# Performance work log

Measured on AMD Instinct MI355X. Metric: run time of the kernel, lower is better.

## Reference

```python
import jax, jax.numpy as jnp
import numpy as np

SCALE = 4.0
GRID = 64
B, T, A, C = 4, 256, 3, 13
F = 5 + C  # x,y,z,r,conf,cls...


def setup_inputs() -> dict:
    key = jax.random.key(0)
    k1, k2, k3, k4, k5 = jax.random.split(key, 5)
    p = jax.random.normal(k1, (B, A, GRID, GRID, GRID, F), dtype=jnp.float32)
    xyz = jax.random.uniform(k2, (B, T, 3), minval=4.0, maxval=SCALE * GRID - 4.0)
    r = jax.random.uniform(k3, (B, T, 1), minval=6.0, maxval=20.0)
    conf = (jax.random.uniform(k4, (B, T, 1)) < 0.6).astype(jnp.float32)
    cls = jax.nn.one_hot(jax.random.randint(k5, (B, T), 0, C), C, dtype=jnp.float32)
    targets = jnp.concatenate([xyz, r, conf, cls], axis=-1)  # [B,T,18]
    anchor = jnp.array([[[8.0], [12.0], [16.0]]], dtype=jnp.float32)  # [1,A,1]
    return {"p": p, "targets": targets, "anchor": anchor}


def _bce(logits, t):
    # BCEWithLogitsLoss (pos_weight=1), elementwise
    return t * jax.nn.softplus(-logits) + (1.0 - t) * jax.nn.softplus(logits)


def _eiou(box1, box2, eps=1e-7):
    # boxes are (x,y,z,r): axis-aligned cubes of side r centered at xyz (3D EIoU)
    c1, r1 = box1[:, :3], box1[:, 3]
    c2, r2 = box2[:, :3], box2[:, 3]
    h1, h2 = r1[:, None] * 0.5, r2[:, None] * 0.5
    lo = jnp.maximum(c1 - h1, c2 - h2)
    hi = jnp.minimum(c1 + h1, c2 + h2)
    inter = jnp.prod(jnp.clip(hi - lo, 0.0), axis=-1)
    union = r1 ** 3 + r2 ** 3 - inter + eps
    iou = inter / union
    clo = jnp.minimum(c1 - h1, c2 - h2)
    chi = jnp.maximum(c1 + h1, c2 + h2)
    cdim = chi - clo  # enclosing box per-axis extent
    rho2 = jnp.sum((c1 - c2) ** 2, axis=-1)
    c2diag = jnp.sum(cdim ** 2, axis=-1) + eps
    size_pen = jnp.sum(((r1 - r2) ** 2)[:, None] / (cdim ** 2 + eps), axis=-1)
    return iou - rho2 / c2diag - size_pen


def reference(p, targets, anchor):
    Bs, An, K, J, I, Fd = p.shape
    Cn = Fd - 5
    g, gr = 0.5, 0.0
    Tn = targets.shape[1]
    n = Bs * Tn
    x = targets.reshape(n, Fd)
    b0 = jnp.repeat(jnp.arange(Bs), Tn)
    conf_m = x[:, 4] > 0.5
    anchor_norm = anchor[0] / SCALE  # [A,1]
    gxyzr = x[:, :4] / SCALE
    rn = gxyzr[:, 3]
    ratio = rn[None, :] / anchor_norm  # [A,n]
    aok = jnp.maximum(ratio, 1.0 / ratio) < 4.0
    gxyz = gxyzr[:, :3]
    gdim = jnp.array([K, J, I], dtype=p.dtype)  # gain[1:]
    gxyz_i = gdim - gxyz
    m1 = (gxyz % 1.0 < g) & (gxyz > 1.0)
    m2 = (gxyz_i % 1.0 < g) & (gxyz_i > 1.0)
    fm = jnp.stack([jnp.ones_like(m1[:, 0]), m1[:, 0], m1[:, 1], m1[:, 2], m2[:, 0], m2[:, 1], m2[:, 2]])  # [7,n]
    off = jnp.array([[0, 0, 0], [1, 0, 0], [0, 1, 0], [0, 0, 1], [-1, 0, 0], [0, -1, 0], [0, 0, -1]], dtype=p.dtype) * g
    valid = (conf_m[None, None, :] & aok[None, :, :] & fm[:, None, :]).reshape(-1)  # [7*A*n]
    bidx = jnp.broadcast_to(b0[None, None, :], (7, An, n)).reshape(-1)
    aidx = jnp.broadcast_to(jnp.arange(An)[None, :, None], (7, An, n)).reshape(-1)
    gxyz_c = jnp.broadcast_to(gxyz[None, None], (7, An, n, 3))
    off_c = jnp.broadcast_to(off[:, None, None, :], (7, An, n, 3))
    gijk_f = jnp.trunc(jax.lax.stop_gradient(gxyz_c - off_c))  # torch .long() truncates
    gijk = gijk_f.astype(jnp.int32).reshape(-1, 3)
    gi = jnp.clip(gijk[:, 0], 0, I - 1)
    gj = jnp.clip(gijk[:, 1], 0, J - 1)
    gk = jnp.clip(gijk[:, 2], 0, K - 1)
    tbox = jnp.concatenate([(gxyz_c - gijk_f).reshape(-1, 3), jnp.broadcast_to(rn[None, None, :], (7, An, n)).reshape(-1, 1)], axis=1)
    anchors = anchor_norm[aidx]  # [N,1]
    tcls = jnp.broadcast_to(x[None, None, :, 5:], (7, An, n, Cn)).reshape(-1, Cn)
    pred = p[bidx, aidx, gk, gj, gi]  # [N,F]
    pxyz = jax.nn.sigmoid(pred[:, :3]) * 2.0 - 0.5
    pr = (jax.nn.sigmoid(pred[:, 3:4]) * 2.0) ** 2 * anchors
    pbox = jnp.concatenate([pxyz, pr], axis=1)
    ei = _eiou(pbox, tbox)
    w = valid.astype(p.dtype)
    nv = jnp.maximum(jnp.sum(w), 1.0)
    loss_bbox = jnp.sum(w * (1.0 - ei)) / nv  # masked mean == torch mean over filtered rows
    iou_d = jax.lax.stop_gradient(jnp.clip(ei, 0.0))
    objv = (1.0 - gr) + gr * iou_d  # gr=0 -> 1.0
    tobj = jnp.zeros((Bs, An, K, J, I), dtype=p.dtype).at[bidx, aidx, gk, gj, gi].max(w * objv)
    loss_cls = jnp.sum(w[:, None] * _bce(pred[:, 5:], tcls)) / (nv * Cn)
    loss_obj = jnp.mean(_bce(p[..., 4], tobj))
    lb = loss_bbox * 1.0
    lo = loss_obj * 20.0
    lc = loss_cls * 10.0
    return ((lb + lo + lc) * Bs, lo, lc)
```

## Files before the change

### kernel.cpp

```cpp
#include <hip/hip_runtime.h>
#include <math.h>

#define NTGT   1024
#define NCAND  (21 * NTGT)
#define NCBLK  (NCAND / 256)
#define NCELL  (4 * 3 * 64 * 64 * 64)
#define BITW   (NCELL / 32)
#define NBLK   2048

__device__ __forceinline__ float softplusf(float x) {
    return fmaxf(x, 0.0f) + __logf(1.0f + __expf(-fabsf(x)));
}
__device__ __forceinline__ float sigmoidf(float x) {
    return 1.0f / (1.0f + __expf(-x));
}

__global__ __launch_bounds__(256) void fused_kernel(
    const float* __restrict__ p, const float* __restrict__ tg,
    const float* __restrict__ anchor, float* __restrict__ acc,
    unsigned int* __restrict__ bitmap)
{
    if (blockIdx.x < NCBLK) {
        int idx = blockIdx.x * 256 + threadIdx.x;
        float nv_v = 0.f, bb_v = 0.f, cl_v = 0.f, ob_v = 0.f;
        {
            int t  = idx & (NTGT - 1);
            int oa = idx >> 10;
            int a  = oa % 3;
            int o  = oa / 3;
            const float* x = tg + t * 18;
            float conf = x[4];
            float rn   = x[3] * 0.25f;
            float an   = anchor[a] * 0.25f;
            float ratio = rn / an;
            bool ok = (conf > 0.5f) && (fmaxf(ratio, 1.0f / ratio) < 4.0f);
            float gv[3] = { x[0] * 0.25f, x[1] * 0.25f, x[2] * 0.25f };
            float off[3] = { 0.f, 0.f, 0.f };
            if (o >= 1) {
                if (o <= 3) {
                    int c = o - 1;
                    float v = gv[c];
                    ok = ok && ((v - floorf(v)) < 0.5f) && (v > 1.0f);
                    off[c] = 0.5f;
                } else {
                    int c = o - 4;
                    float vi = 64.0f - gv[c];
                    ok = ok && ((vi - floorf(vi)) < 0.5f) && (vi > 1.0f);
                    off[c] = -0.5f;
                }
            }
            if (ok) {
                float tb[3]; int gq[3];
                #pragma unroll
                for (int c = 0; c < 3; c++) {
                    float f = truncf(gv[c] - off[c]);
                    tb[c] = gv[c] - f;
                    gq[c] = min(max((int)f, 0), 63);
                }
                int b0 = t >> 8;
                unsigned int cell =
                    ((((unsigned)(b0 * 3 + a) * 64u + (unsigned)gq[2]) * 64u
                      + (unsigned)gq[1]) * 64u) + (unsigned)gq[0];
                const float* pp = p + (size_t)cell * 18u;
                float pd[18];
                #pragma unroll
                for (int f = 0; f < 18; f++) pd[f] = pp[f];

                float c1[3];
                #pragma unroll
                for (int c = 0; c < 3; c++) c1[c] = sigmoidf(pd[c]) * 2.0f - 0.5f;
                float s4 = sigmoidf(pd[3]) * 2.0f;
                float r1 = s4 * s4 * an;
                float r2 = rn;

                float h1 = 0.5f * r1, h2 = 0.5f * r2;
                float inter = 1.f, rho2 = 0.f, c2d = 0.f, spen = 0.f;
                float dr2 = (r1 - r2) * (r1 - r2);
                #pragma unroll
                for (int c = 0; c < 3; c++) {
                    float lo1 = c1[c] - h1, hi1 = c1[c] + h1;
                    float lo2 = tb[c] - h2, hi2 = tb[c] + h2;
                    inter *= fmaxf(fminf(hi1, hi2) - fmaxf(lo1, lo2), 0.f);
                    float cd  = fmaxf(hi1, hi2) - fminf(lo1, lo2);
                    float cd2 = cd * cd;
                    float d   = c1[c] - tb[c];
                    rho2 += d * d;
                    c2d  += cd2;
                    spen += dr2 / (cd2 + 1e-7f);
                }
                float uni = r1 * r1 * r1 + r2 * r2 * r2 - inter + 1e-7f;
                float ei  = inter / uni - rho2 / (c2d + 1e-7f) - spen;

                nv_v = 1.0f;
                bb_v = 1.0f - ei;
                float cl = 0.f;
                #pragma unroll
                for (int c = 0; c < 13; c++) {
                    float l = pd[5 + c];
                    cl += softplusf(l) - x[5 + c] * l;
                }
                cl_v = cl;
                unsigned int old = atomicOr(&bitmap[cell >> 5], 1u << (cell & 31u));
                if (!(old & (1u << (cell & 31u)))) ob_v = pd[4];
            }
        }
        #pragma unroll
        for (int s = 32; s > 0; s >>= 1) {
            nv_v += __shfl_down(nv_v, s, 64);
            bb_v += __shfl_down(bb_v, s, 64);
            cl_v += __shfl_down(cl_v, s, 64);
            ob_v += __shfl_down(ob_v, s, 64);
        }
        if ((threadIdx.x & 63) == 0 && nv_v != 0.f) {
            atomicAdd(&acc[0], nv_v);
            atomicAdd(&acc[1], bb_v);
            atomicAdd(&acc[2], cl_v);
            atomicAdd(&acc[4], ob_v);
        }
    }

    float s = 0.f;
    {
        int i = blockIdx.x * 256 + threadIdx.x;
        #pragma unroll
        for (int it = 0; it < NCELL / (NBLK * 256); it++) {
            s += softplusf(p[(size_t)i * 18u + 4u]);
            i += NBLK * 256;
        }
    }
    #pragma unroll
    for (int sh = 32; sh > 0; sh >>= 1) s += __shfl_down(s, sh, 64);
    __shared__ float sm[4];
    int lane = threadIdx.x & 63, w = threadIdx.x >> 6;
    if (lane == 0) sm[w] = s;
    __syncthreads();
    if (threadIdx.x == 0) {
        atomicAdd(&acc[3], sm[0] + sm[1] + sm[2] + sm[3]);
    }
}

__global__ void final_kernel(const float* __restrict__ acc, float* __restrict__ out)
{
    float nv = fmaxf(acc[0], 1.0f);
    float lb = acc[1] / nv;
    float lc = acc[2] / (nv * 13.0f) * 10.0f;
    float lo = (acc[3] - acc[4]) * (20.0f / (float)NCELL);
    out[0] = (lb + lo + lc) * 4.0f;
    out[1] = lo;
    out[2] = lc;
}

extern "C" void kernel_launch(void* const* d_in, const int* in_sizes, int n_in,
                              void* d_out, int out_size, void* d_ws, size_t ws_size,
                              hipStream_t stream) {
    const float* p       = (const float*)d_in[0];
    const float* targets = (const float*)d_in[1];
    const float* anchor  = (const float*)d_in[2];
    float* out = (float*)d_out;

    float* acc = (float*)d_ws;
    unsigned int* bitmap = (unsigned int*)((char*)d_ws + 32);

    hipMemsetAsync(d_ws, 0, 32 + (size_t)BITW * 4, stream);

    fused_kernel<<<NBLK, 256, 0, stream>>>(p, targets, anchor, acc, bitmap);
    final_kernel<<<1, 1, 0, stream>>>(acc, out);
}
```

Measured before the change: 312.4 us.

## Use cooperative grid sync with LDS bitmaps to drop memset and final kernel

Replaces the global bitmap and memset with a per-(batch,anchor) 32KB shared-memory bitmap in 12 blocks. Each of those blocks loops over all 7 offsets for 256 targets. The kernel now launches cooperatively with 768 blocks and a grid sync, and block 0 does the final reduction, which removes the separate final kernel, the memset and the global atomics. The cost is a grid-wide barrier, a serialized candidate loop in only 12 blocks, and 32KB of LDS per block, which may limit occupancy during the streaming softplus pass.

Result: slower. 413.8 us (+32.5%).

```diff
diff --git a/kernel.cpp b/kernel.cpp
--- a/kernel.cpp
+++ b/kernel.cpp
@@ -1,12 +1,13 @@
 #include <hip/hip_runtime.h>
+#include <hip/hip_cooperative_groups.h>
 #include <math.h>
 
-#define NTGT   1024
-#define NCAND  (21 * NTGT)
-#define NCBLK  (NCAND / 256)
+namespace cg = cooperative_groups;
+
 #define NCELL  (4 * 3 * 64 * 64 * 64)
-#define BITW   (NCELL / 32)
-#define NBLK   2048
+#define NBLK   768
+#define NITER  (NCELL / (NBLK * 256))
+
 
 __device__ __forceinline__ float softplusf(float x) {
     return fmaxf(x, 0.0f) + __logf(1.0f + __expf(-fabsf(x)));
@@ -15,53 +16,48 @@
     return 1.0f / (1.0f + __expf(-x));
 }
 
-__global__ __launch_bounds__(256) void fused_kernel(
+__global__ __launch_bounds__(256, 3) void fused_kernel(
     const float* __restrict__ p, const float* __restrict__ tg,
-    const float* __restrict__ anchor, float* __restrict__ acc,
-    unsigned int* __restrict__ bitmap)
+    const float* __restrict__ anchor, float* __restrict__ out,
+    float* __restrict__ ws)
 {
-    if (blockIdx.x < NCBLK) {
-        int idx = blockIdx.x * 256 + threadIdx.x;
+    __shared__ unsigned int bm[8192];
+    __shared__ float smr[16];
+
+    if (blockIdx.x < 12) {
+        for (int i = threadIdx.x; i < 8192; i += 256) bm[i] = 0u;
+        __syncthreads();
+
+        const int    b0 = (int)blockIdx.x / 3;
+        const int    a  = (int)blockIdx.x % 3;
+        const float* x  = tg + (size_t)(b0 * 256 + (int)threadIdx.x) * 18u;
+        const float conf  = x[4];
+        const float rn    = x[3] * 0.25f;
+        const float an    = anchor[a] * 0.25f;
+        const float ratio = rn / an;
+        const bool  base_ok = (conf > 0.5f) && (fmaxf(ratio, 1.0f / ratio) < 4.0f);
+        const float gv0 = x[0] * 0.25f, gv1 = x[1] * 0.25f, gv2 = x[2] * 0.25f;
+
         float nv_v = 0.f, bb_v = 0.f, cl_v = 0.f, ob_v = 0.f;
-        {
-            int t  = idx & (NTGT - 1);
-            int oa = idx >> 10;
-            int a  = oa % 3;
-            int o  = oa / 3;
-            const float* x = tg + t * 18;
-            float conf = x[4];
-            float rn   = x[3] * 0.25f;
-            float an   = anchor[a] * 0.25f;
-            float ratio = rn / an;
-            bool ok = (conf > 0.5f) && (fmaxf(ratio, 1.0f / ratio) < 4.0f);
-            float gv[3] = { x[0] * 0.25f, x[1] * 0.25f, x[2] * 0.25f };
-            float off[3] = { 0.f, 0.f, 0.f };
-            if (o >= 1) {
-                if (o <= 3) {
-                    int c = o - 1;
-                    float v = gv[c];
-                    ok = ok && ((v - floorf(v)) < 0.5f) && (v > 1.0f);
-                    off[c] = 0.5f;
-                } else {
-                    int c = o - 4;
-                    float vi = 64.0f - gv[c];
-                    ok = ok && ((vi - floorf(vi)) < 0.5f) && (vi > 1.0f);
-                    off[c] = -0.5f;
-                }
-            }
+
+        #pragma unroll
+        for (int o = 0; o < 7; o++) {
+            bool ok = base_ok;
+            float off0 = 0.f, off1 = 0.f, off2 = 0.f;
+            if (o == 1) { ok = ok && ((gv0 - floorf(gv0)) < 0.5f) && (gv0 > 1.0f); off0 =  0.5f; }
+            if (o == 2) { ok = ok && ((gv1 - floorf(gv1)) < 0.5f) && (gv1 > 1.0f); off1 =  0.5f; }
+            if (o == 3) { ok = ok && ((gv2 - floorf(gv2)) < 0.5f) && (gv2 > 1.0f); off2 =  0.5f; }
+            if (o == 4) { float vi = 64.0f - gv0; ok = ok && ((vi - floorf(vi)) < 0.5f) && (vi > 1.0f); off0 = -0.5f; }
+            if (o == 5) { float vi = 64.0f - gv1; ok = ok && ((vi - floorf(vi)) < 0.5f) && (vi > 1.0f); off1 = -0.5f; }
+            if (o == 6) { float vi = 64.0f - gv2; ok = ok && ((vi - floorf(vi)) < 0.5f) && (vi > 1.0f); off2 = -0.5f; }
             if (ok) {
-                float tb[3]; int gq[3];
-                #pragma unroll
-                for (int c = 0; c < 3; c++) {
-                    float f = truncf(gv[c] - off[c]);
-                    tb[c] = gv[c] - f;
-                    gq[c] = min(max((int)f, 0), 63);
-                }
-                int b0 = t >> 8;
-                unsigned int cell =
-                    ((((unsigned)(b0 * 3 + a) * 64u + (unsigned)gq[2]) * 64u
-                      + (unsigned)gq[1]) * 64u) + (unsigned)gq[0];
-                const float* pp = p + (size_t)cell * 18u;
+                float f0 = truncf(gv0 - off0), f1 = truncf(gv1 - off1), f2 = truncf(gv2 - off2);
+                float tb[3] = { gv0 - f0, gv1 - f1, gv2 - f2 };
+                int gq0 = min(max((int)f0, 0), 63);
+                int gq1 = min(max((int)f1, 0), 63);
+                int gq2 = min(max((int)f2, 0), 63);
+                unsigned int cellL = (((unsigned)gq2 * 64u + (unsigned)gq1) * 64u) + (unsigned)gq0;
+                const float* pp = p + ((size_t)blockIdx.x * 262144u + cellL) * 18u;
                 float pd[18];
                 #pragma unroll
                 for (int f = 0; f < 18; f++) pd[f] = pp[f];
@@ -91,78 +87,105 @@
                 float uni = r1 * r1 * r1 + r2 * r2 * r2 - inter + 1e-7f;
                 float ei  = inter / uni - rho2 / (c2d + 1e-7f) - spen;
 
-                nv_v = 1.0f;
-                bb_v = 1.0f - ei;
+                nv_v += 1.0f;
+                bb_v += 1.0f - ei;
                 float cl = 0.f;
                 #pragma unroll
                 for (int c = 0; c < 13; c++) {
                     float l = pd[5 + c];
                     cl += softplusf(l) - x[5 + c] * l;
                 }
-                cl_v = cl;
-                unsigned int old = atomicOr(&bitmap[cell >> 5], 1u << (cell & 31u));
-                if (!(old & (1u << (cell & 31u)))) ob_v = pd[4];
+                cl_v += cl;
+                unsigned int bit = 1u << (cellL & 31u);
+                unsigned int old = atomicOr(&bm[cellL >> 5], bit);
+                if (!(old & bit)) ob_v += pd[4];
             }
         }
         #pragma unroll
-        for (int s = 32; s > 0; s >>= 1) {
-            nv_v += __shfl_down(nv_v, s, 64);
-            bb_v += __shfl_down(bb_v, s, 64);
-            cl_v += __shfl_down(cl_v, s, 64);
-            ob_v += __shfl_down(ob_v, s, 64);
+        for (int sh = 32; sh > 0; sh >>= 1) {
+            nv_v += __shfl_down(nv_v, sh, 64);
+            bb_v += __shfl_down(bb_v, sh, 64);
+            cl_v += __shfl_down(cl_v, sh, 64);
+            ob_v += __shfl_down(ob_v, sh, 64);
         }
-        if ((threadIdx.x & 63) == 0 && nv_v != 0.f) {
-            atomicAdd(&acc[0], nv_v);
-            atomicAdd(&acc[1], bb_v);
-            atomicAdd(&acc[2], cl_v);
-            atomicAdd(&acc[4], ob_v);
+        int lane = threadIdx.x & 63, w = threadIdx.x >> 6;
+        if (lane == 0) {
+            smr[w * 4 + 0] = nv_v; smr[w * 4 + 1] = bb_v;
+            smr[w * 4 + 2] = cl_v; smr[w * 4 + 3] = ob_v;
+        }
+        __syncthreads();
+        if (threadIdx.x == 0) {
+            #pragma unroll
+            for (int k = 0; k < 4; k++) {
+                float v = smr[k] + smr[4 + k] + smr[8 + k] + smr[12 + k];
+                __hip_atomic_store(&ws[blockIdx.x * 4 + k], v,
+                                   __ATOMIC_RELAXED, __HIP_MEMORY_SCOPE_AGENT);
+            }
         }
     }
 
     float s = 0.f;
     {
-        int i = blockIdx.x * 256 + threadIdx.x;
+        size_t i = (size_t)blockIdx.x * 256u + threadIdx.x;
         #pragma unroll
-        for (int it = 0; it < NCELL / (NBLK * 256); it++) {
-            s += softplusf(p[(size_t)i * 18u + 4u]);
-            i += NBLK * 256;
+        for (int it = 0; it < NITER; it++) {
+            s += softplusf(p[i * 18u + 4u]);
+            i += (size_t)NBLK * 256u;
         }
     }
     #pragma unroll
     for (int sh = 32; sh > 0; sh >>= 1) s += __shfl_down(s, sh, 64);
-    __shared__ float sm[4];
-    int lane = threadIdx.x & 63, w = threadIdx.x >> 6;
-    if (lane == 0) sm[w] = s;
+    __syncthreads();
+    {
+        int lane = threadIdx.x & 63, w = threadIdx.x >> 6;
+        if (lane == 0) smr[w] = s;
+    }
     __syncthreads();
     if (threadIdx.x == 0) {
-        atomicAdd(&acc[3], sm[0] + sm[1] + sm[2] + sm[3]);
+        __hip_atomic_store(&ws[64 + blockIdx.x], smr[0] + smr[1] + smr[2] + smr[3],
+                           __ATOMIC_RELAXED, __HIP_MEMORY_SCOPE_AGENT);
     }
-}
 
-__global__ void final_kernel(const float* __restrict__ acc, float* __restrict__ out)
-{
-    float nv = fmaxf(acc[0], 1.0f);
-    float lb = acc[1] / nv;
-    float lc = acc[2] / (nv * 13.0f) * 10.0f;
-    float lo = (acc[3] - acc[4]) * (20.0f / (float)NCELL);
-    out[0] = (lb + lo + lc) * 4.0f;
-    out[1] = lo;
-    out[2] = lc;
+    cg::this_grid().sync();
+
+    if (blockIdx.x == 0 && threadIdx.x < 64) {
+        float s2 = 0.f;
+        #pragma unroll
+        for (int j = 0; j < NBLK / 64; j++)
+            s2 += __hip_atomic_load(&ws[64 + (int)threadIdx.x + j * 64],
+                                    __ATOMIC_RELAXED, __HIP_MEMORY_SCOPE_AGENT);
+        #pragma unroll
+        for (int sh = 32; sh > 0; sh >>= 1) s2 += __shfl_down(s2, sh, 64);
+        if (threadIdx.x == 0) {
+            float nv = 0.f, bb = 0.f, cl = 0.f, ob = 0.f;
+            for (int q = 0; q < 12; q++) {
+                nv += __hip_atomic_load(&ws[q * 4 + 0], __ATOMIC_RELAXED, __HIP_MEMORY_SCOPE_AGENT);
+                bb += __hip_atomic_load(&ws[q * 4 + 1], __ATOMIC_RELAXED, __HIP_MEMORY_SCOPE_AGENT);
+                cl += __hip_atomic_load(&ws[q * 4 + 2], __ATOMIC_RELAXED, __HIP_MEMORY_SCOPE_AGENT);
+                ob += __hip_atomic_load(&ws[q * 4 + 3], __ATOMIC_RELAXED, __HIP_MEMORY_SCOPE_AGENT);
+            }
+            nv = fmaxf(nv, 1.0f);
+            float lb = bb / nv;
+            float lc = cl / (nv * 13.0f) * 10.0f;
+            float lo = (s2 - ob) * (20.0f / (float)NCELL);
+            out[0] = (lb + lo + lc) * 4.0f;
+            out[1] = lo;
+            out[2] = lc;
+        }
+    }
 }
 
 extern "C" void kernel_launch(void* const* d_in, const int* in_sizes, int n_in,
                               void* d_out, int out_size, void* d_ws, size_t ws_size,
                               hipStream_t stream) {
+    (void)in_sizes; (void)n_in; (void)out_size; (void)ws_size;
     const float* p       = (const float*)d_in[0];
     const float* targets = (const float*)d_in[1];
     const float* anchor  = (const float*)d_in[2];
     float* out = (float*)d_out;
+    float* ws  = (float*)d_ws;
 
-    float* acc = (float*)d_ws;
-    unsigned int* bitmap = (unsigned int*)((char*)d_ws + 32);
-
-    hipMemsetAsync(d_ws, 0, 32 + (size_t)BITW * 4, stream);
-
-    fused_kernel<<<NBLK, 256, 0, stream>>>(p, targets, anchor, acc, bitmap);
-    final_kernel<<<1, 1, 0, stream>>>(acc, out);
+    void* args[] = { (void*)&p, (void*)&targets, (void*)&anchor, (void*)&out, (void*)&ws };
+    hipLaunchCooperativeKernel((const void*)fused_kernel, dim3(NBLK), dim3(256),
+                               args, 0, stream);
 }
```
